# Optimization experiments

Hardware: AMD Instinct MI355X
Metric: run time of the kernel (lower is better)

## Reference

```python
import jax, jax.numpy as jnp
import numpy as np

PI = float(np.pi)


def _layernorm(x, g, b, eps=1e-5):
    mu = jnp.mean(x, axis=-1, keepdims=True)
    var = jnp.var(x, axis=-1, keepdims=True)
    return (x - mu) * jax.lax.rsqrt(var + eps) * g + b


def setup_inputs() -> dict:
    key = jax.random.key(0)
    B, L, D, P = 4, 2048, 256, 32
    ks = jax.random.split(key, 16)

    def lin_w(k, fi, fo):
        return (jax.random.normal(k, (fi, fo), dtype=jnp.float32) / np.sqrt(fi)).astype(jnp.float32)

    inp = {
        'x': jax.random.normal(ks[0], (B, L, D), dtype=jnp.float32),
        'pos_phases': jax.random.normal(ks[1], (L, P), dtype=jnp.float32) * PI,
        'w_mem1v': lin_w(ks[2], D, P), 'b_mem1v': jnp.zeros((P,), jnp.float32),
        'w_mem1o': lin_w(ks[3], P, D), 'b_mem1o': jnp.zeros((D,), jnp.float32),
        'w_off': lin_w(ks[4], D + P, P), 'b_off': jnp.zeros((P,), jnp.float32),
        'w_key': lin_w(ks[5], D, P), 'b_key': jnp.zeros((P,), jnp.float32),
        'w_val': lin_w(ks[6], D, D), 'b_val': jnp.zeros((D,), jnp.float32),
        'w_sk1': lin_w(ks[7], 2 * D, D), 'b_sk1': jnp.zeros((D,), jnp.float32),
        'w_sk2': lin_w(ks[8], D, P), 'b_sk2': jnp.zeros((P,), jnp.float32),
        'w_gate': lin_w(ks[9], D, 1), 'b_gate': jnp.zeros((1,), jnp.float32),
        'ln_g': jnp.ones((D,), jnp.float32), 'ln_b': jnp.zeros((D,), jnp.float32),
        'w_out': lin_w(ks[10], D, D), 'b_out': jnp.zeros((D,), jnp.float32),
    }
    return inp


def reference(x, pos_phases, w_mem1v, b_mem1v, w_mem1o, b_mem1o, w_off, b_off,
              w_key, b_key, w_val, b_val, w_sk1, b_sk1, w_sk2, b_sk2,
              w_gate, b_gate, ln_g, ln_b, w_out, b_out):
    B, L, D = x.shape
    P = pos_phases.shape[-1]

    pos_cos = jnp.cos(pos_phases)  # [L,P]
    pos_sin = jnp.sin(pos_phases)

    # Memory 1: flat [B,L,P] phasor cumulative memory
    v1 = x @ w_mem1v + b_mem1v                       # [B,L,P]
    mem1_cos = jnp.cumsum(pos_cos[None] * v1, axis=1)
    mem1_sin = jnp.cumsum(pos_sin[None] * v1, axis=1)

    offset_input = jnp.concatenate([x, jnp.broadcast_to(pos_phases[None], (B, L, P))], axis=-1)
    offset = jnp.tanh(offset_input @ w_off + b_off) * PI
    oc, os = jnp.cos(offset), jnp.sin(offset)
    query_cos = pos_cos[None] * oc - pos_sin[None] * os
    query_sin = pos_sin[None] * oc + pos_cos[None] * os
    pos_ret = (mem1_cos * query_cos + mem1_sin * query_sin) / np.sqrt(P)
    pos_out = pos_ret @ w_mem1o + b_mem1o            # [B,L,D]

    # Memory 2: full [B,L,P,D] phasor KV cumulative memory
    key_phases = jnp.tanh(x @ w_key + b_key) * PI    # [B,L,P]
    key_cos, key_sin = jnp.cos(key_phases), jnp.sin(key_phases)
    values = x @ w_val + b_val                       # [B,L,D]
    store_gate = jax.nn.sigmoid(x @ w_gate + b_gate) # [B,L,1]

    positions = jnp.arange(1, L + 1, dtype=x.dtype)[None, :, None]
    context_avg = jnp.cumsum(x, axis=1) / positions
    h = jax.nn.gelu(jnp.concatenate([x, context_avg], axis=-1) @ w_sk1 + b_sk1, approximate=False)
    storage_phases = jnp.tanh(h @ w_sk2 + b_sk2) * PI  # [B,L,P]

    gated_v = values * store_gate                    # [B,L,D]
    kv_mem_cos = jnp.cumsum(jnp.cos(storage_phases)[..., None] * gated_v[:, :, None, :], axis=1)  # [B,L,P,D]
    kv_mem_sin = jnp.cumsum(jnp.sin(storage_phases)[..., None] * gated_v[:, :, None, :], axis=1)

    gate_cumsum = jnp.clip(jnp.cumsum(store_gate, axis=1), 1.0, None)  # [B,L,1]
    kv_retrieved = jnp.einsum('blpd,blp->bld', kv_mem_cos, key_cos) + \
                   jnp.einsum('blpd,blp->bld', kv_mem_sin, key_sin)
    kv_retrieved = kv_retrieved / (jnp.sqrt(gate_cumsum) * np.sqrt(P))

    combined = pos_out + kv_retrieved
    return x + _layernorm(combined, ln_g, ln_b) @ w_out + b_out
```

## Files before the change

kernel.cpp:

```cpp
#include <hip/hip_runtime.h>
#include <hip/hip_bf16.h>

constexpr int B_ = 4;
constexpr int L_ = 2048;
constexpr int D_ = 256;
constexpr int P_ = 32;
constexpr int CL = 32;
constexpr int NC = L_ / CL;

#define PI_F 3.14159265358979323846f
#define INV_SQRT_P 0.17677669529663687f

typedef __attribute__((ext_vector_type(8))) short short8_t;
typedef __attribute__((ext_vector_type(4))) float floatx4;

static __device__ inline short f2bf(float f) {
  unsigned int u;
  __builtin_memcpy(&u, &f, 4);
  unsigned int r = (u + 0x7fffu + ((u >> 16) & 1u)) >> 16;
  return (short)r;
}

__global__ void wprep(const float* __restrict__ x, const float* __restrict__ pos,
                      const float* __restrict__ w_val, const float* __restrict__ w_mem1v,
                      const float* __restrict__ w_off, const float* __restrict__ b_off,
                      const float* __restrict__ w_key, const float* __restrict__ w_gate,
                      const float* __restrict__ w_sk1, const float* __restrict__ w_out,
                      const float* __restrict__ w_sk2, const float* __restrict__ w_mem1o,
                      short* __restrict__ WA, short* __restrict__ W1,
                      short* __restrict__ WO, short* __restrict__ W2T,
                      short* __restrict__ W1OT,
                      short* __restrict__ xbf, float* __restrict__ poff) {
  int blk = blockIdx.x, tid = threadIdx.x;
  if (blk < 384) {
    int idx = blk * 256 + tid;
    int n = idx >> 8, k = idx & 255;
    float v;
    if (n < 256) v = w_val[k * 256 + n];
    else if (n < 288) v = w_mem1v[k * 32 + (n - 256)];
    else if (n < 320) v = w_off[k * 32 + (n - 288)];
    else if (n < 352) v = w_key[k * 32 + (n - 320)];
    else if (n == 352) v = w_gate[k];
    else v = 0.f;
    WA[idx] = f2bf(v);
  } else if (blk < 896) {
    int idx = (blk - 384) * 256 + tid;
    int n = idx >> 9, k = idx & 511;
    W1[idx] = f2bf(w_sk1[k * 256 + n]);
  } else if (blk < 1152) {
    int idx = (blk - 896) * 256 + tid;
    int n = idx >> 8, k = idx & 255;
    WO[idx] = f2bf(w_out[k * 256 + n]);
  } else if (blk < 1184) {
    int idx = (blk - 1152) * 256 + tid;
    int p = idx >> 8, k = idx & 255;
    W2T[idx] = f2bf(w_sk2[k * 32 + p]);
  } else if (blk < 1216) {
    int idx = (blk - 1184) * 256 + tid;
    int d = idx >> 5, p = idx & 31;
    W1OT[idx] = f2bf(w_mem1o[p * 256 + d]);
  } else if (blk < 3264) {
    int idx = ((blk - 1216) * 256 + tid) * 4;
    float4 v = *(const float4*)&x[idx];
    short4 o;
    o.x = f2bf(v.x); o.y = f2bf(v.y); o.z = f2bf(v.z); o.w = f2bf(v.w);
    *(short4*)&xbf[idx] = o;
  } else {
    int idx = (blk - 3264) * 256 + tid;
    int l = idx >> 5, p = idx & 31;
    float a = b_off[p];
    for (int j = 0; j < 32; ++j) a += pos[l * 32 + j] * w_off[(256 + j) * 32 + p];
    poff[idx] = a;
  }
}

template <int KTILES, int NBLK, int MODE>
__global__ __launch_bounds__(256) void gemm_k(const short* __restrict__ A0,
                                              const short* __restrict__ A1,
                                              const short* __restrict__ W,
                                              const float* __restrict__ bias,
                                              const float* __restrict__ xres,
                                              float* __restrict__ outf,
                                              short* __restrict__ outb) {
  __shared__ short As[64][136];
  __shared__ short Bs[64][136];
  int tid = threadIdx.x;
  int mg = blockIdx.x / NBLK, ng = blockIdx.x % NBLK;
  int tok0 = mg * 64, n0 = ng * 64;
  int lane = tid & 63, w = tid >> 6;
  int mw = (w & 1) * 32, nw = (w >> 1) * 32;
  floatx4 acc[2][2] = {{{0.f, 0.f, 0.f, 0.f}, {0.f, 0.f, 0.f, 0.f}},
                       {{0.f, 0.f, 0.f, 0.f}, {0.f, 0.f, 0.f, 0.f}}};
  int r2 = tid >> 4, c8 = tid & 15;
  int ml = lane & 15, kq = (lane >> 4) * 8;
  const int K = KTILES * 128;

  for (int kt = 0; kt < KTILES; ++kt) {
    const short* Asrc;
    int cb;
    if (KTILES == 4) {
      Asrc = (kt < 2) ? A0 : A1;
      cb = (kt & 1) * 128;
    } else {
      Asrc = A0;
      cb = kt * 128;
    }
#pragma unroll
    for (int pass = 0; pass < 4; ++pass) {
      int row = pass * 16 + r2;
      *(short8_t*)&As[row][c8 * 8] =
          *(const short8_t*)&Asrc[(tok0 + row) * 256 + cb + c8 * 8];
      *(short8_t*)&Bs[row][c8 * 8] =
          *(const short8_t*)&W[(n0 + row) * K + kt * 128 + c8 * 8];
    }
    __syncthreads();
#pragma unroll
    for (int s = 0; s < 4; ++s) {
      short8_t a0 = *(short8_t*)&As[mw + ml][s * 32 + kq];
      short8_t a1 = *(short8_t*)&As[mw + 16 + ml][s * 32 + kq];
      short8_t b0 = *(short8_t*)&Bs[nw + ml][s * 32 + kq];
      short8_t b1 = *(short8_t*)&Bs[nw + 16 + ml][s * 32 + kq];
      acc[0][0] = __builtin_amdgcn_mfma_f32_16x16x32_bf16(a0, b0, acc[0][0], 0, 0, 0);
      acc[0][1] = __builtin_amdgcn_mfma_f32_16x16x32_bf16(a0, b1, acc[0][1], 0, 0, 0);
      acc[1][0] = __builtin_amdgcn_mfma_f32_16x16x32_bf16(a1, b0, acc[1][0], 0, 0, 0);
      acc[1][1] = __builtin_amdgcn_mfma_f32_16x16x32_bf16(a1, b1, acc[1][1], 0, 0, 0);
    }
    __syncthreads();
  }
  int col = lane & 15, rq = (lane >> 4) * 4;
#pragma unroll
  for (int nt = 0; nt < 2; ++nt) {
    int n = n0 + nw + nt * 16 + col;
    float bv = (MODE == 0) ? 0.f : bias[n];
#pragma unroll
    for (int mt = 0; mt < 2; ++mt) {
#pragma unroll
      for (int rg = 0; rg < 4; ++rg) {
        int tok = tok0 + mw + mt * 16 + rq + rg;
        float v = acc[mt][nt][rg] + bv;
        if (MODE == 0) {
          outf[tok * 384 + n] = v;
        } else if (MODE == 1) {
          float g = 0.5f * v * (1.f + erff(v * 0.70710678118654752f));
          outb[tok * 256 + n] = f2bf(g);
        } else {
          outf[tok * 256 + n] = xres[tok * 256 + n] + v;
        }
      }
    }
  }
}

__global__ void kernelA3(const float* __restrict__ Y, const float* __restrict__ pos,
                         const float* __restrict__ poff, const float* __restrict__ b_mem1v,
                         const float* __restrict__ b_key, const float* __restrict__ b_gate,
                         const float* __restrict__ b_val,
                         float* __restrict__ m1c, float* __restrict__ m1s,
                         float* __restrict__ qc, float* __restrict__ qs,
                         short* __restrict__ K2bf, short* __restrict__ gvT,
                         float* __restrict__ sg) {
  __shared__ float gsh[8];
  int tid = threadIdx.x;
  int tok0 = blockIdx.x * 8;
  int t = tid >> 5, p = tid & 31;
  int tok = tok0 + t, l = tok & (L_ - 1);
  float gate = 1.f / (1.f + expf(-(Y[tok * 384 + 352] + b_gate[0])));
  if (p == 0) {
    sg[tok] = gate;
    gsh[t] = gate;
  }
  float v1 = Y[tok * 384 + 256 + p] + b_mem1v[p];
  float ph = pos[l * 32 + p];
  float pc = cosf(ph), ps = sinf(ph);
  int idx = tok * 32 + p;
  m1c[idx] = pc * v1;
  m1s[idx] = ps * v1;
  float off = tanhf(Y[tok * 384 + 288 + p] + poff[l * 32 + p]) * PI_F;
  float oc = cosf(off), os = sinf(off);
  qc[idx] = pc * oc - ps * os;
  qs[idx] = ps * oc + pc * os;
  float kp = tanhf(Y[tok * 384 + 320 + p] + b_key[p]) * PI_F;
  K2bf[tok * 64 + p] = f2bf(cosf(kp));
  K2bf[tok * 64 + 32 + p] = f2bf(sinf(kp));
  __syncthreads();
  {
    int b = tok0 / L_;
    int l0 = tok0 & (L_ - 1);
    int bc = b * NC + (l0 >> 5);
    int tl0 = l0 & 31;
    short sv[8];
#pragma unroll
    for (int tt = 0; tt < 8; ++tt)
      sv[tt] = f2bf((Y[(tok0 + tt) * 384 + tid] + b_val[tid]) * gsh[tt]);
    *(short8_t*)&gvT[(bc * 256 + tid) * 32 + tl0] = *(short8_t*)sv;
  }
}

__global__ void scan_all(float* __restrict__ m1c, float* __restrict__ m1s,
                         float* __restrict__ sg, const float* __restrict__ x,
                         short* __restrict__ ctxbf) {
  int blk = blockIdx.x;
  int tid = threadIdx.x, lane = tid & 63, wid = tid >> 6;
  __shared__ float wsum[4];
  float carry = 0.f;
  float* arr = nullptr;
  const float* src = nullptr;
  int base, inner, mode;
  if (blk < 256) {
    arr = (blk < 128) ? m1c : m1s;
    int row = blk & 127;
    int b = row >> 5, r = row & 31;
    base = b * L_ * P_ + r;
    inner = P_;
    mode = 0;
    src = arr;
  } else if (blk < 260) {
    arr = sg;
    base = (blk - 256) * L_;
    inner = 1;
    mode = 0;
    src = arr;
  } else {
    int row = blk - 260;
    int b = row >> 8, r = row & 255;
    base = b * L_ * D_ + r;
    inner = D_;
    mode = 1;
    src = x;
  }
  for (int t0 = 0; t0 < L_; t0 += 256) {
    int l = t0 + tid;
    float v = src[base + l * inner];
#pragma unroll
    for (int off = 1; off < 64; off <<= 1) {
      float n = __shfl_up(v, off, 64);
      if (lane >= off) v += n;
    }
    if (lane == 63) wsum[wid] = v;
    __syncthreads();
    float add = carry;
    for (int w = 0; w < wid; ++w) add += wsum[w];
    float res = v + add;
    if (mode == 0) arr[base + l * inner] = res;
    else ctxbf[base + l * inner] = f2bf(res / (float)(l + 1));
    carry += wsum[0] + wsum[1] + wsum[2] + wsum[3];
    __syncthreads();
  }
}

__global__ __launch_bounds__(256) void kernelCD(const short* __restrict__ hs,
                                                const short* __restrict__ W2T,
                                                const float* __restrict__ b_sk2,
                                                const short* __restrict__ gvT,
                                                short* __restrict__ SPbf,
                                                float* __restrict__ U) {
  __shared__ __align__(16) short SPL[2][64][40];
  int tid = threadIdx.x;
  int tok0 = blockIdx.x * 64;
  int lane = tid & 63, w = tid >> 6;
  int ml = lane & 15, quad = lane >> 4, kq = quad * 8;
  int m0 = w * 16;
  floatx4 pacc[2] = {};
#pragma unroll
  for (int s = 0; s < 8; ++s) {
    short8_t a = *(const short8_t*)&hs[(tok0 + m0 + ml) * 256 + s * 32 + kq];
    short8_t b0 = *(const short8_t*)&W2T[ml * 256 + s * 32 + kq];
    short8_t b1 = *(const short8_t*)&W2T[(16 + ml) * 256 + s * 32 + kq];
    pacc[0] = __builtin_amdgcn_mfma_f32_16x16x32_bf16(a, b0, pacc[0], 0, 0, 0);
    pacc[1] = __builtin_amdgcn_mfma_f32_16x16x32_bf16(a, b1, pacc[1], 0, 0, 0);
  }
  int cl = w >> 1;
#pragma unroll
  for (int nt = 0; nt < 2; ++nt) {
    int p = nt * 16 + ml;
    float bs = b_sk2[p];
#pragma unroll
    for (int r = 0; r < 4; ++r) {
      int tok = tok0 + m0 + quad * 4 + r;
      float sp = tanhf(pacc[nt][r] + bs) * PI_F;
      short c = f2bf(cosf(sp)), s = f2bf(sinf(sp));
      int tl = (w & 1) * 16 + quad * 4 + r;
      SPL[cl][p][tl] = c;
      SPL[cl][32 + p][tl] = s;
      SPbf[tok * 64 + p] = c;
      SPbf[tok * 64 + 32 + p] = s;
    }
  }
  __syncthreads();
  int c2 = w & 1, dbase = (w >> 1) * 128;
  int bc = blockIdx.x * 2 + c2;
  short8_t a[4];
#pragma unroll
  for (int mt = 0; mt < 4; ++mt) a[mt] = *(short8_t*)&SPL[c2][mt * 16 + ml][kq];
#pragma unroll
  for (int dp = 0; dp < 2; ++dp) {
    floatx4 acc[4][4] = {};
#pragma unroll
    for (int nt = 0; nt < 4; ++nt) {
      short8_t b = *(const short8_t*)&gvT[(bc * 256 + dbase + dp * 64 + nt * 16 + ml) * 32 + kq];
#pragma unroll
      for (int mt = 0; mt < 4; ++mt)
        acc[mt][nt] = __builtin_amdgcn_mfma_f32_16x16x32_bf16(a[mt], b, acc[mt][nt], 0, 0, 0);
    }
#pragma unroll
    for (int mt = 0; mt < 4; ++mt)
#pragma unroll
      for (int nt = 0; nt < 4; ++nt)
#pragma unroll
        for (int r = 0; r < 4; ++r) {
          int q = mt * 16 + quad * 4 + r;
          int d = dbase + dp * 64 + nt * 16 + ml;
          U[(bc * 64 + q) * 256 + d] = acc[mt][nt][r];
        }
  }
}

__global__ void kernelE(float* __restrict__ U) {
  int tid = blockIdx.x * 256 + threadIdx.x;
  int d = tid % D_;
  int q = (tid / D_) % 64;
  int b = tid / (D_ * 64);
  int base = ((b * NC) * 64 + q) * D_ + d;
  const int cs = 64 * D_;
  float run = 0.f;
  for (int c0 = 0; c0 < NC; c0 += 8) {
    float v[8];
#pragma unroll
    for (int j = 0; j < 8; ++j) v[j] = U[base + (c0 + j) * cs];
#pragma unroll
    for (int j = 0; j < 8; ++j) {
      U[base + (c0 + j) * cs] = run;
      run += v[j];
    }
  }
}

__global__ __launch_bounds__(256) void kernelFG(const float* __restrict__ U,
                                                const short* __restrict__ SPbf,
                                                const short* __restrict__ K2bf,
                                                const short* __restrict__ gvT,
                                                const float* __restrict__ sgc,
                                                const float* __restrict__ m1c,
                                                const float* __restrict__ m1s,
                                                const float* __restrict__ qc,
                                                const float* __restrict__ qs,
                                                const short* __restrict__ W1OT,
                                                const float* __restrict__ b_mem1o,
                                                const float* __restrict__ ln_g,
                                                const float* __restrict__ ln_b,
                                                short* __restrict__ cbn) {
  __shared__ __align__(16) short Ub[256][40];
  __shared__ __align__(16) short SL[32][40];
  __shared__ __align__(16) short PR[32][40];
  __shared__ float CMB[32][260];
  __shared__ float scl[32], mu_s[32], rs_s[32];
  int tid = threadIdx.x;
  int bc = blockIdx.x;
  int lbase = bc * CL;
  if (tid < 32) scl[tid] = rsqrtf(fmaxf(sgc[lbase + tid], 1.f)) * INV_SQRT_P;
  for (int it = 0; it < 8; ++it) {
    int idx = it * 256 + tid;
    int q = idx >> 6, d4 = idx & 63;
    float4 v = *(const float4*)&U[(bc * 64 + q) * 256 + d4 * 4];
    Ub[d4 * 4 + 0][q] = f2bf(v.x);
    Ub[d4 * 4 + 1][q] = f2bf(v.y);
    Ub[d4 * 4 + 2][q] = f2bf(v.z);
    Ub[d4 * 4 + 3][q] = f2bf(v.w);
  }
  for (int it = 0; it < 4; ++it) {
    int i = it * 256 + tid;
    int g = lbase * 32 + i;
    PR[i >> 5][i & 31] = f2bf((m1c[g] * qc[g] + m1s[g] * qs[g]) * INV_SQRT_P);
  }
  __syncthreads();
  int lane = tid & 63, w = tid >> 6;
  int ml = lane & 15, quad = lane >> 4, kq = quad * 8;
  floatx4 acc[2][4] = {};
  short8_t ka0 = *(const short8_t*)&K2bf[(lbase + ml) * 64 + kq];
  short8_t ka1 = *(const short8_t*)&K2bf[(lbase + 16 + ml) * 64 + kq];
  short8_t kb0 = *(const short8_t*)&K2bf[(lbase + ml) * 64 + 32 + kq];
  short8_t kb1 = *(const short8_t*)&K2bf[(lbase + 16 + ml) * 64 + 32 + kq];
#pragma unroll
  for (int nt = 0; nt < 4; ++nt) {
    short8_t b = *(short8_t*)&Ub[w * 64 + nt * 16 + ml][kq];
    acc[0][nt] = __builtin_amdgcn_mfma_f32_16x16x32_bf16(ka0, b, acc[0][nt], 0, 0, 0);
    acc[1][nt] = __builtin_amdgcn_mfma_f32_16x16x32_bf16(ka1, b, acc[1][nt], 0, 0, 0);
  }
  if (w == 0) {
    floatx4 sacc[2][2] = {};
#pragma unroll
    for (int ks2 = 0; ks2 < 2; ++ks2) {
      short8_t a0 = (ks2 == 0) ? ka0 : kb0;
      short8_t a1 = (ks2 == 0) ? ka1 : kb1;
      short8_t b0 = *(const short8_t*)&SPbf[(lbase + ml) * 64 + ks2 * 32 + kq];
      short8_t b1 = *(const short8_t*)&SPbf[(lbase + 16 + ml) * 64 + ks2 * 32 + kq];
      sacc[0][0] = __builtin_amdgcn_mfma_f32_16x16x32_bf16(a0, b0, sacc[0][0], 0, 0, 0);
      sacc[0][1] = __builtin_amdgcn_mfma_f32_16x16x32_bf16(a0, b1, sacc[0][1], 0, 0, 0);
      sacc[1][0] = __builtin_amdgcn_mfma_f32_16x16x32_bf16(a1, b0, sacc[1][0], 0, 0, 0);
      sacc[1][1] = __builtin_amdgcn_mfma_f32_16x16x32_bf16(a1, b1, sacc[1][1], 0, 0, 0);
    }
#pragma unroll
    for (int mt = 0; mt < 2; ++mt)
#pragma unroll
      for (int nt = 0; nt < 2; ++nt)
#pragma unroll
        for (int r = 0; r < 4; ++r) {
          int trow = mt * 16 + quad * 4 + r;
          int scol = nt * 16 + ml;
          float v = (scol <= trow) ? sacc[mt][nt][r] : 0.f;
          SL[trow][scol] = f2bf(v);
        }
  }
  __syncthreads();
  for (int it = 0; it < 8; ++it) {
    int idx = it * 256 + tid;
    int q = idx >> 6, d4 = idx & 63;
    float4 v = *(const float4*)&U[(bc * 64 + 32 + q) * 256 + d4 * 4];
    Ub[d4 * 4 + 0][q] = f2bf(v.x);
    Ub[d4 * 4 + 1][q] = f2bf(v.y);
    Ub[d4 * 4 + 2][q] = f2bf(v.z);
    Ub[d4 * 4 + 3][q] = f2bf(v.w);
  }
  __syncthreads();
#pragma unroll
  for (int nt = 0; nt < 4; ++nt) {
    short8_t b = *(short8_t*)&Ub[w * 64 + nt * 16 + ml][kq];
    acc[0][nt] = __builtin_amdgcn_mfma_f32_16x16x32_bf16(kb0, b, acc[0][nt], 0, 0, 0);
    acc[1][nt] = __builtin_amdgcn_mfma_f32_16x16x32_bf16(kb1, b, acc[1][nt], 0, 0, 0);
  }
  {
    short8_t a0 = *(short8_t*)&SL[ml][kq];
    short8_t a1 = *(short8_t*)&SL[16 + ml][kq];
#pragma unroll
    for (int nt = 0; nt < 4; ++nt) {
      short8_t b = *(const short8_t*)&gvT[(bc * 256 + w * 64 + nt * 16 + ml) * 32 + kq];
      acc[0][nt] = __builtin_amdgcn_mfma_f32_16x16x32_bf16(a0, b, acc[0][nt], 0, 0, 0);
      acc[1][nt] = __builtin_amdgcn_mfma_f32_16x16x32_bf16(a1, b, acc[1][nt], 0, 0, 0);
    }
  }
  floatx4 macc[2][4] = {};
  {
    short8_t a0 = *(short8_t*)&PR[ml][kq];
    short8_t a1 = *(short8_t*)&PR[16 + ml][kq];
#pragma unroll
    for (int nt = 0; nt < 4; ++nt) {
      short8_t b = *(const short8_t*)&W1OT[(w * 64 + nt * 16 + ml) * 32 + kq];
      macc[0][nt] = __builtin_amdgcn_mfma_f32_16x16x32_bf16(a0, b, macc[0][nt], 0, 0, 0);
      macc[1][nt] = __builtin_amdgcn_mfma_f32_16x16x32_bf16(a1, b, macc[1][nt], 0, 0, 0);
    }
  }
#pragma unroll
  for (int mt = 0; mt < 2; ++mt)
#pragma unroll
    for (int nt = 0; nt < 4; ++nt) {
      int d = w * 64 + nt * 16 + ml;
      float bm = b_mem1o[d];
#pragma unroll
      for (int r = 0; r < 4; ++r) {
        int t = mt * 16 + quad * 4 + r;
        CMB[t][d] = acc[mt][nt][r] * scl[t] + macc[mt][nt][r] + bm;
      }
    }
  __syncthreads();
  {
    int t = tid >> 3, g = tid & 7;
    float s = 0.f, s2 = 0.f;
#pragma unroll
    for (int j = 0; j < 32; ++j) {
      float v = CMB[t][g + j * 8];
      s += v;
      s2 += v * v;
    }
#pragma unroll
    for (int m = 1; m < 8; m <<= 1) {
      s += __shfl_xor(s, m, 64);
      s2 += __shfl_xor(s2, m, 64);
    }
    if (g == 0) {
      float mu = s / (float)D_;
      float var = s2 / (float)D_ - mu * mu;
      mu_s[t] = mu;
      rs_s[t] = rsqrtf(var + 1e-5f);
    }
  }
  __syncthreads();
  {
    float lg = ln_g[tid], lb = ln_b[tid];
#pragma unroll
    for (int t = 0; t < 32; ++t)
      cbn[(lbase + t) * 256 + tid] = f2bf((CMB[t][tid] - mu_s[t]) * rs_s[t] * lg + lb);
  }
}

extern "C" void kernel_launch(void* const* d_in, const int* in_sizes, int n_in,
                              void* d_out, int out_size, void* d_ws, size_t ws_size,
                              hipStream_t stream) {
  const float* x = (const float*)d_in[0];
  const float* pos = (const float*)d_in[1];
  const float* w_mem1v = (const float*)d_in[2];
  const float* b_mem1v = (const float*)d_in[3];
  const float* w_mem1o = (const float*)d_in[4];
  const float* b_mem1o = (const float*)d_in[5];
  const float* w_off = (const float*)d_in[6];
  const float* b_off = (const float*)d_in[7];
  const float* w_key = (const float*)d_in[8];
  const float* b_key = (const float*)d_in[9];
  const float* w_val = (const float*)d_in[10];
  const float* b_val = (const float*)d_in[11];
  const float* w_sk1 = (const float*)d_in[12];
  const float* b_sk1 = (const float*)d_in[13];
  const float* w_sk2 = (const float*)d_in[14];
  const float* b_sk2 = (const float*)d_in[15];
  const float* w_gate = (const float*)d_in[16];
  const float* b_gate = (const float*)d_in[17];
  const float* ln_g = (const float*)d_in[18];
  const float* ln_b = (const float*)d_in[19];
  const float* w_out = (const float*)d_in[20];
  const float* b_out = (const float*)d_in[21];
  float* out = (float*)d_out;
  float* ws = (float*)d_ws;

  const int BLP = B_ * L_ * P_;
  const int BLD = B_ * L_ * D_;
  float* m1c = ws;
  float* m1s = m1c + BLP;
  float* qc = m1s + BLP;
  float* qs = qc + BLP;
  float* sg = qs + BLP;
  float* poff = sg + B_ * L_;
  float* Y = poff + L_ * P_;
  float* U = Y;
  short* xbf = (short*)(U + (size_t)B_ * NC * 64 * D_);
  short* cbn = xbf;
  short* ctxbf = xbf + BLD;
  short* hs = ctxbf + BLD;
  short* gvT = hs + BLD;
  short* K2bf = gvT + BLD;
  short* SPbf = K2bf + B_ * L_ * 64;
  short* WA = SPbf + B_ * L_ * 64;
  short* W1 = WA + 384 * 256;
  short* WO = W1 + 256 * 512;
  short* W2T = WO + 256 * 256;
  short* W1OT = W2T + 32 * 256;

  wprep<<<3520, 256, 0, stream>>>(x, pos, w_val, w_mem1v, w_off, b_off, w_key, w_gate,
                                  w_sk1, w_out, w_sk2, w_mem1o, WA, W1, WO, W2T, W1OT,
                                  xbf, poff);
  gemm_k<2, 6, 0><<<128 * 6, 256, 0, stream>>>(xbf, nullptr, WA, nullptr, nullptr, Y, nullptr);
  kernelA3<<<(B_ * L_) / 8, 256, 0, stream>>>(Y, pos, poff, b_mem1v, b_key, b_gate, b_val,
                                              m1c, m1s, qc, qs, K2bf, gvT, sg);
  scan_all<<<260 + B_ * D_, 256, 0, stream>>>(m1c, m1s, sg, x, ctxbf);
  gemm_k<4, 4, 1><<<128 * 4, 256, 0, stream>>>(xbf, ctxbf, W1, b_sk1, nullptr, nullptr, hs);
  kernelCD<<<(B_ * L_) / 64, 256, 0, stream>>>(hs, W2T, b_sk2, gvT, SPbf, U);
  kernelE<<<(B_ * 64 * D_) / 256, 256, 0, stream>>>(U);
  kernelFG<<<B_ * NC, 256, 0, stream>>>(U, SPbf, K2bf, gvT, sg, m1c, m1s, qc, qs,
                                        W1OT, b_mem1o, ln_g, ln_b, cbn);
  gemm_k<2, 4, 2><<<128 * 4, 256, 0, stream>>>(cbn, nullptr, WO, b_out, x, out, nullptr);
}
```

Measured before the change: 193.8 us.

## Store intermediates in bf16 and transposed layouts, split context scan into chunks

The first GEMM now writes Y in bf16, and the chunk-state tensor U is stored as bf16 transposed (UT), so kernelFG reads MFMA operands straight from global memory instead of transposing through shared memory. The m1 cos/sin buffers are stored transposed so the scan reads contiguously. The strided per-column cumulative context average is replaced by a chunk-sum pass plus a separate kernelCtx that rescans each chunk. These changes cut memory traffic and uncoalesced accesses, at the cost of bf16 rounding in the carried prefix states, an extra kernel launch, and a quadratic chunk-prefix loop in kernelCtx.

```diff
diff --git a/kernel.cpp b/kernel.cpp
--- a/kernel.cpp
+++ b/kernel.cpp
@@ -19,6 +19,12 @@
   __builtin_memcpy(&u, &f, 4);
   unsigned int r = (u + 0x7fffu + ((u >> 16) & 1u)) >> 16;
   return (short)r;
+}
+static __device__ inline float bf2f(short s) {
+  unsigned int u = ((unsigned int)(unsigned short)s) << 16;
+  float f;
+  __builtin_memcpy(&f, &u, 4);
+  return f;
 }
 
 __global__ void wprep(const float* __restrict__ x, const float* __restrict__ pos,
@@ -139,7 +145,7 @@
         int tok = tok0 + mw + mt * 16 + rq + rg;
         float v = acc[mt][nt][rg] + bv;
         if (MODE == 0) {
-          outf[tok * 384 + n] = v;
+          outb[tok * 384 + n] = f2bf(v);
         } else if (MODE == 1) {
           float g = 0.5f * v * (1.f + erff(v * 0.70710678118654752f));
           outb[tok * 256 + n] = f2bf(g);
@@ -151,11 +157,11 @@
   }
 }
 
-__global__ void kernelA3(const float* __restrict__ Y, const float* __restrict__ pos,
+__global__ void kernelA3(const short* __restrict__ Ybf, const float* __restrict__ pos,
                          const float* __restrict__ poff, const float* __restrict__ b_mem1v,
                          const float* __restrict__ b_key, const float* __restrict__ b_gate,
                          const float* __restrict__ b_val,
-                         float* __restrict__ m1c, float* __restrict__ m1s,
+                         float* __restrict__ m1cT, float* __restrict__ m1sT,
                          float* __restrict__ qc, float* __restrict__ qs,
                          short* __restrict__ K2bf, short* __restrict__ gvT,
                          float* __restrict__ sg) {
@@ -164,73 +170,69 @@
   int tok0 = blockIdx.x * 8;
   int t = tid >> 5, p = tid & 31;
   int tok = tok0 + t, l = tok & (L_ - 1);
-  float gate = 1.f / (1.f + expf(-(Y[tok * 384 + 352] + b_gate[0])));
+  int b = tok >> 11;
+  float gate = 1.f / (1.f + expf(-(bf2f(Ybf[tok * 384 + 352]) + b_gate[0])));
   if (p == 0) {
     sg[tok] = gate;
     gsh[t] = gate;
   }
-  float v1 = Y[tok * 384 + 256 + p] + b_mem1v[p];
+  float v1 = bf2f(Ybf[tok * 384 + 256 + p]) + b_mem1v[p];
   float ph = pos[l * 32 + p];
   float pc = cosf(ph), ps = sinf(ph);
+  int idxT = (b * 32 + p) * L_ + l;
+  m1cT[idxT] = pc * v1;
+  m1sT[idxT] = ps * v1;
+  float off = tanhf(bf2f(Ybf[tok * 384 + 288 + p]) + poff[l * 32 + p]) * PI_F;
+  float oc = cosf(off), os = sinf(off);
   int idx = tok * 32 + p;
-  m1c[idx] = pc * v1;
-  m1s[idx] = ps * v1;
-  float off = tanhf(Y[tok * 384 + 288 + p] + poff[l * 32 + p]) * PI_F;
-  float oc = cosf(off), os = sinf(off);
   qc[idx] = pc * oc - ps * os;
   qs[idx] = ps * oc + pc * os;
-  float kp = tanhf(Y[tok * 384 + 320 + p] + b_key[p]) * PI_F;
+  float kp = tanhf(bf2f(Ybf[tok * 384 + 320 + p]) + b_key[p]) * PI_F;
   K2bf[tok * 64 + p] = f2bf(cosf(kp));
   K2bf[tok * 64 + 32 + p] = f2bf(sinf(kp));
   __syncthreads();
   {
-    int b = tok0 / L_;
     int l0 = tok0 & (L_ - 1);
-    int bc = b * NC + (l0 >> 5);
+    int bc = (tok0 >> 11) * NC + (l0 >> 5);
     int tl0 = l0 & 31;
     short sv[8];
 #pragma unroll
     for (int tt = 0; tt < 8; ++tt)
-      sv[tt] = f2bf((Y[(tok0 + tt) * 384 + tid] + b_val[tid]) * gsh[tt]);
+      sv[tt] = f2bf((bf2f(Ybf[(tok0 + tt) * 384 + tid]) + b_val[tid]) * gsh[tt]);
     *(short8_t*)&gvT[(bc * 256 + tid) * 32 + tl0] = *(short8_t*)sv;
   }
 }
 
-__global__ void scan_all(float* __restrict__ m1c, float* __restrict__ m1s,
+__global__ void scan_all(float* __restrict__ m1cT, float* __restrict__ m1sT,
                          float* __restrict__ sg, const float* __restrict__ x,
-                         short* __restrict__ ctxbf) {
+                         float* __restrict__ ctxsum) {
   int blk = blockIdx.x;
-  int tid = threadIdx.x, lane = tid & 63, wid = tid >> 6;
+  int tid = threadIdx.x;
+  if (blk >= 260) {
+    int c2 = blk - 260;
+    int b = c2 >> 6, ch = c2 & 63;
+    int xb = (b * L_ + ch * 32) * 256 + tid;
+    float s = 0.f;
+#pragma unroll 8
+    for (int i = 0; i < 32; ++i) s += x[xb + i * 256];
+    ctxsum[c2 * 256 + tid] = s;
+    return;
+  }
+  int lane = tid & 63, wid = tid >> 6;
   __shared__ float wsum[4];
   float carry = 0.f;
-  float* arr = nullptr;
-  const float* src = nullptr;
-  int base, inner, mode;
+  float* arr;
+  int base;
   if (blk < 256) {
-    arr = (blk < 128) ? m1c : m1s;
-    int row = blk & 127;
-    int b = row >> 5, r = row & 31;
-    base = b * L_ * P_ + r;
-    inner = P_;
-    mode = 0;
-    src = arr;
-  } else if (blk < 260) {
+    arr = (blk < 128) ? m1cT : m1sT;
+    base = (blk & 127) * L_;
+  } else {
     arr = sg;
     base = (blk - 256) * L_;
-    inner = 1;
-    mode = 0;
-    src = arr;
-  } else {
-    int row = blk - 260;
-    int b = row >> 8, r = row & 255;
-    base = b * L_ * D_ + r;
-    inner = D_;
-    mode = 1;
-    src = x;
   }
   for (int t0 = 0; t0 < L_; t0 += 256) {
     int l = t0 + tid;
-    float v = src[base + l * inner];
+    float v = arr[base + l];
 #pragma unroll
     for (int off = 1; off < 64; off <<= 1) {
       float n = __shfl_up(v, off, 64);
@@ -240,11 +242,26 @@
     __syncthreads();
     float add = carry;
     for (int w = 0; w < wid; ++w) add += wsum[w];
-    float res = v + add;
-    if (mode == 0) arr[base + l * inner] = res;
-    else ctxbf[base + l * inner] = f2bf(res / (float)(l + 1));
+    arr[base + l] = v + add;
     carry += wsum[0] + wsum[1] + wsum[2] + wsum[3];
     __syncthreads();
+  }
+}
+
+__global__ void kernelCtx(const float* __restrict__ x, const float* __restrict__ ctxsum,
+                          short* __restrict__ ctxbf) {
+  int c2 = blockIdx.x;
+  int b = c2 >> 6, ch = c2 & 63;
+  int tid = threadIdx.x;
+  float run = 0.f;
+  int sb = b * 64 * 256 + tid;
+  for (int c = 0; c < ch; ++c) run += ctxsum[sb + c * 256];
+  int xb = (b * L_ + ch * 32) * 256 + tid;
+#pragma unroll 8
+  for (int i = 0; i < 32; ++i) {
+    run += x[xb + i * 256];
+    int l = ch * 32 + i;
+    ctxbf[xb + i * 256] = f2bf(run / (float)(l + 1));
   }
 }
 
@@ -253,7 +270,7 @@
                                                 const float* __restrict__ b_sk2,
                                                 const short* __restrict__ gvT,
                                                 short* __restrict__ SPbf,
-                                                float* __restrict__ U) {
+                                                short* __restrict__ UT) {
   __shared__ __align__(16) short SPL[2][64][40];
   int tid = threadIdx.x;
   int tok0 = blockIdx.x * 64;
@@ -310,38 +327,38 @@
         for (int r = 0; r < 4; ++r) {
           int q = mt * 16 + quad * 4 + r;
           int d = dbase + dp * 64 + nt * 16 + ml;
-          U[(bc * 64 + q) * 256 + d] = acc[mt][nt][r];
+          UT[(bc * 256 + d) * 64 + q] = f2bf(acc[mt][nt][r]);
         }
   }
 }
 
-__global__ void kernelE(float* __restrict__ U) {
+__global__ void kernelE(short* __restrict__ UT) {
   int tid = blockIdx.x * 256 + threadIdx.x;
-  int d = tid % D_;
-  int q = (tid / D_) % 64;
-  int b = tid / (D_ * 64);
-  int base = ((b * NC) * 64 + q) * D_ + d;
-  const int cs = 64 * D_;
+  int q = tid & 63;
+  int d = (tid >> 6) & 255;
+  int b = tid >> 14;
+  int base = ((b * NC) * 256 + d) * 64 + q;
+  const int cs = 256 * 64;
   float run = 0.f;
   for (int c0 = 0; c0 < NC; c0 += 8) {
-    float v[8];
-#pragma unroll
-    for (int j = 0; j < 8; ++j) v[j] = U[base + (c0 + j) * cs];
+    short v[8];
+#pragma unroll
+    for (int j = 0; j < 8; ++j) v[j] = UT[base + (c0 + j) * cs];
 #pragma unroll
     for (int j = 0; j < 8; ++j) {
-      U[base + (c0 + j) * cs] = run;
-      run += v[j];
-    }
-  }
-}
-
-__global__ __launch_bounds__(256) void kernelFG(const float* __restrict__ U,
+      UT[base + (c0 + j) * cs] = f2bf(run);
+      run += bf2f(v[j]);
+    }
+  }
+}
+
+__global__ __launch_bounds__(256) void kernelFG(const short* __restrict__ UT,
                                                 const short* __restrict__ SPbf,
                                                 const short* __restrict__ K2bf,
                                                 const short* __restrict__ gvT,
                                                 const float* __restrict__ sgc,
-                                                const float* __restrict__ m1c,
-                                                const float* __restrict__ m1s,
+                                                const float* __restrict__ m1cT,
+                                                const float* __restrict__ m1sT,
                                                 const float* __restrict__ qc,
                                                 const float* __restrict__ qs,
                                                 const short* __restrict__ W1OT,
@@ -349,7 +366,6 @@
                                                 const float* __restrict__ ln_g,
                                                 const float* __restrict__ ln_b,
                                                 short* __restrict__ cbn) {
-  __shared__ __align__(16) short Ub[256][40];
   __shared__ __align__(16) short SL[32][40];
   __shared__ __align__(16) short PR[32][40];
   __shared__ float CMB[32][260];
@@ -357,22 +373,15 @@
   int tid = threadIdx.x;
   int bc = blockIdx.x;
   int lbase = bc * CL;
+  int bb = bc >> 6, lloc = (bc & 63) * 32;
   if (tid < 32) scl[tid] = rsqrtf(fmaxf(sgc[lbase + tid], 1.f)) * INV_SQRT_P;
-  for (int it = 0; it < 8; ++it) {
-    int idx = it * 256 + tid;
-    int q = idx >> 6, d4 = idx & 63;
-    float4 v = *(const float4*)&U[(bc * 64 + q) * 256 + d4 * 4];
-    Ub[d4 * 4 + 0][q] = f2bf(v.x);
-    Ub[d4 * 4 + 1][q] = f2bf(v.y);
-    Ub[d4 * 4 + 2][q] = f2bf(v.z);
-    Ub[d4 * 4 + 3][q] = f2bf(v.w);
-  }
   for (int it = 0; it < 4; ++it) {
     int i = it * 256 + tid;
-    int g = lbase * 32 + i;
-    PR[i >> 5][i & 31] = f2bf((m1c[g] * qc[g] + m1s[g] * qs[g]) * INV_SQRT_P);
-  }
-  __syncthreads();
+    int p = i >> 5, t = i & 31;
+    int gT = (bb * 32 + p) * L_ + lloc + t;
+    int g = (lbase + t) * 32 + p;
+    PR[t][p] = f2bf((m1cT[gT] * qc[g] + m1sT[gT] * qs[g]) * INV_SQRT_P);
+  }
   int lane = tid & 63, w = tid >> 6;
   int ml = lane & 15, quad = lane >> 4, kq = quad * 8;
   floatx4 acc[2][4] = {};
@@ -382,7 +391,7 @@
   short8_t kb1 = *(const short8_t*)&K2bf[(lbase + 16 + ml) * 64 + 32 + kq];
 #pragma unroll
   for (int nt = 0; nt < 4; ++nt) {
-    short8_t b = *(short8_t*)&Ub[w * 64 + nt * 16 + ml][kq];
+    short8_t b = *(const short8_t*)&UT[(bc * 256 + w * 64 + nt * 16 + ml) * 64 + kq];
     acc[0][nt] = __builtin_amdgcn_mfma_f32_16x16x32_bf16(ka0, b, acc[0][nt], 0, 0, 0);
     acc[1][nt] = __builtin_amdgcn_mfma_f32_16x16x32_bf16(ka1, b, acc[1][nt], 0, 0, 0);
   }
@@ -412,19 +421,9 @@
         }
   }
   __syncthreads();
-  for (int it = 0; it < 8; ++it) {
-    int idx = it * 256 + tid;
-    int q = idx >> 6, d4 = idx & 63;
-    float4 v = *(const float4*)&U[(bc * 64 + 32 + q) * 256 + d4 * 4];
-    Ub[d4 * 4 + 0][q] = f2bf(v.x);
-    Ub[d4 * 4 + 1][q] = f2bf(v.y);
-    Ub[d4 * 4 + 2][q] = f2bf(v.z);
-    Ub[d4 * 4 + 3][q] = f2bf(v.w);
-  }
-  __syncthreads();
 #pragma unroll
   for (int nt = 0; nt < 4; ++nt) {
-    short8_t b = *(short8_t*)&Ub[w * 64 + nt * 16 + ml][kq];
+    short8_t b = *(const short8_t*)&UT[(bc * 256 + w * 64 + nt * 16 + ml) * 64 + 32 + kq];
     acc[0][nt] = __builtin_amdgcn_mfma_f32_16x16x32_bf16(kb0, b, acc[0][nt], 0, 0, 0);
     acc[1][nt] = __builtin_amdgcn_mfma_f32_16x16x32_bf16(kb1, b, acc[1][nt], 0, 0, 0);
   }
@@ -522,15 +521,16 @@
 
   const int BLP = B_ * L_ * P_;
   const int BLD = B_ * L_ * D_;
-  float* m1c = ws;
-  float* m1s = m1c + BLP;
-  float* qc = m1s + BLP;
+  float* m1cT = ws;
+  float* m1sT = m1cT + BLP;
+  float* qc = m1sT + BLP;
   float* qs = qc + BLP;
   float* sg = qs + BLP;
   float* poff = sg + B_ * L_;
-  float* Y = poff + L_ * P_;
-  float* U = Y;
-  short* xbf = (short*)(U + (size_t)B_ * NC * 64 * D_);
+  float* ctxsum = poff + L_ * P_;
+  short* Ybf = (short*)(ctxsum + B_ * 64 * 256);
+  short* UT = Ybf;
+  short* xbf = UT + (size_t)B_ * NC * 256 * 64;
   short* cbn = xbf;
   short* ctxbf = xbf + BLD;
   short* hs = ctxbf + BLD;
@@ -546,14 +546,15 @@
   wprep<<<3520, 256, 0, stream>>>(x, pos, w_val, w_mem1v, w_off, b_off, w_key, w_gate,
                                   w_sk1, w_out, w_sk2, w_mem1o, WA, W1, WO, W2T, W1OT,
                                   xbf, poff);
-  gemm_k<2, 6, 0><<<128 * 6, 256, 0, stream>>>(xbf, nullptr, WA, nullptr, nullptr, Y, nullptr);
-  kernelA3<<<(B_ * L_) / 8, 256, 0, stream>>>(Y, pos, poff, b_mem1v, b_key, b_gate, b_val,
-                                              m1c, m1s, qc, qs, K2bf, gvT, sg);
-  scan_all<<<260 + B_ * D_, 256, 0, stream>>>(m1c, m1s, sg, x, ctxbf);
+  gemm_k<2, 6, 0><<<128 * 6, 256, 0, stream>>>(xbf, nullptr, WA, nullptr, nullptr, nullptr, Ybf);
+  kernelA3<<<(B_ * L_) / 8, 256, 0, stream>>>(Ybf, pos, poff, b_mem1v, b_key, b_gate, b_val,
+                                              m1cT, m1sT, qc, qs, K2bf, gvT, sg);
+  scan_all<<<516, 256, 0, stream>>>(m1cT, m1sT, sg, x, ctxsum);
+  kernelCtx<<<256, 256, 0, stream>>>(x, ctxsum, ctxbf);
   gemm_k<4, 4, 1><<<128 * 4, 256, 0, stream>>>(xbf, ctxbf, W1, b_sk1, nullptr, nullptr, hs);
-  kernelCD<<<(B_ * L_) / 64, 256, 0, stream>>>(hs, W2T, b_sk2, gvT, SPbf, U);
-  kernelE<<<(B_ * 64 * D_) / 256, 256, 0, stream>>>(U);
-  kernelFG<<<B_ * NC, 256, 0, stream>>>(U, SPbf, K2bf, gvT, sg, m1c, m1s, qc, qs,
+  kernelCD<<<(B_ * L_) / 64, 256, 0, stream>>>(hs, W2T, b_sk2, gvT, SPbf, UT);
+  kernelE<<<256, 256, 0, stream>>>(UT);
+  kernelFG<<<B_ * NC, 256, 0, stream>>>(UT, SPbf, K2bf, gvT, sg, m1cT, m1sT, qc, qs,
                                         W1OT, b_mem1o, ln_g, ln_b, cbn);
   gemm_k<2, 4, 2><<<128 * 4, 256, 0, stream>>>(cbn, nullptr, WO, b_out, x, out, nullptr);
 }
```

New measurement: 190.6 us. No clear change (-1.7%).
